# Optimization experiments

Measured on AMD Instinct MI355X. Metric: run time of the kernel, lower is better.

The kernel has to match this reference:

```python
import jax, jax.numpy as jnp
import numpy as np

N_HEAD = 16


def setup_inputs() -> dict:
    key = jax.random.key(0)
    ks = jax.random.split(key, 5)
    B, T, D_IN, D = 2, 2048, 1152, 1024
    s_in = 1.0 / np.sqrt(D_IN)
    s_d = 1.0 / np.sqrt(D)
    return {
        "xp": jax.random.normal(ks[0], (B, T, D_IN), jnp.float32),
        "Wq": jax.random.normal(ks[1], (D_IN, D), jnp.float32) * s_in,
        "bq": jnp.zeros((D,), jnp.float32),
        "Wk": jax.random.normal(ks[2], (D_IN, D), jnp.float32) * s_in,
        "bk": jnp.zeros((D,), jnp.float32),
        "Wv": jax.random.normal(ks[3], (D_IN, D), jnp.float32) * s_in,
        "bv": jnp.zeros((D,), jnp.float32),
        "Wp": jax.random.normal(ks[4], (D, D), jnp.float32) * s_d,
        "bp": jnp.zeros((D,), jnp.float32),
    }


def reference(xp, Wq, bq, Wk, bk, Wv, bv, Wp, bp):
    B, T, _ = xp.shape
    D = Wq.shape[1]
    hd = D // N_HEAD  # head dim
    # q, k, v projections -> [B, H, T, hd]
    def split_heads(t):
        return t.reshape(B, T, N_HEAD, hd).transpose(0, 2, 1, 3)
    q = split_heads(xp @ Wq + bq)
    k = split_heads(xp @ Wk + bk)
    v = split_heads(xp @ Wv + bv)
    scale = 1.0 / np.sqrt(hd).astype(np.float32)
    att = jnp.einsum("bhqd,bhkd->bhqk", q, k) * scale  # [B,H,T,T]
    causal = jnp.tril(jnp.ones((T, T), bool))
    att = jnp.where(causal[None, None], att, -jnp.inf)
    att = jax.nn.softmax(att, axis=-1)
    y = jnp.einsum("bhqk,bhkd->bhqd", att, v)  # [B,H,T,hd]
    y = y.transpose(0, 2, 1, 3).reshape(B, T, D)
    return y @ Wp + bp
```

## Files before the change

### kernel.cpp

```cpp
#include <hip/hip_runtime.h>
#include <hip/hip_bf16.h>

typedef __attribute__((ext_vector_type(8))) short bf16x8;
typedef __attribute__((ext_vector_type(4))) short bf16x4;
typedef __attribute__((ext_vector_type(4))) float f32x4;
typedef __attribute__((ext_vector_type(2))) unsigned int u32x2;

__device__ __forceinline__ void gload_lds16(const void* g, void* l) {
    __builtin_amdgcn_global_load_lds(
        (const __attribute__((address_space(1))) unsigned int*)g,
        (__attribute__((address_space(3))) unsigned int*)l, 16, 0, 0);
}

__device__ __forceinline__ unsigned int pk2(float x, float y) {
    union { __hip_bfloat16 h[2]; unsigned int u; } z;
    z.h[0] = __float2bfloat16(x); z.h[1] = __float2bfloat16(y);
    return z.u;
}

__device__ __forceinline__ f32x4 mfma_16x16x16(bf16x4 a, bf16x4 b, f32x4 c) {
#if __has_builtin(__builtin_amdgcn_mfma_f32_16x16x16bf16_1k)
    return __builtin_amdgcn_mfma_f32_16x16x16bf16_1k(a, b, c, 0, 0, 0);
#else
    f32x4 d = c;
    asm volatile("v_mfma_f32_16x16x16_bf16 %0, %1, %2, %0" : "+v"(d) : "v"(a), "v"(b));
    return d;
#endif
}

__global__ void k_cvt_bf16(const float* __restrict__ x, __hip_bfloat16* __restrict__ o, int n8) {
    int i = blockIdx.x * 256 + threadIdx.x;
    if (i >= n8) return;
    const float4* xp = (const float4*)(x + (size_t)i * 8);
    float4 a = xp[0], b = xp[1];
    union { __hip_bfloat16 h[8]; uint4 u; } tu;
    tu.h[0] = __float2bfloat16(a.x); tu.h[1] = __float2bfloat16(a.y);
    tu.h[2] = __float2bfloat16(a.z); tu.h[3] = __float2bfloat16(a.w);
    tu.h[4] = __float2bfloat16(b.x); tu.h[5] = __float2bfloat16(b.y);
    tu.h[6] = __float2bfloat16(b.z); tu.h[7] = __float2bfloat16(b.w);
    *(uint4*)(o + (size_t)i * 8) = tu.u;
}

__global__ void k_tr3(const float* __restrict__ s0, const float* __restrict__ s1,
                      const float* __restrict__ s2, __hip_bfloat16* __restrict__ dst,
                      int K, int N) {
    __shared__ float tile[32][33];
    const float* src = (blockIdx.z == 0) ? s0 : ((blockIdx.z == 1) ? s1 : s2);
    __hip_bfloat16* d = dst + (size_t)blockIdx.z * N * K;
    int n0 = blockIdx.x * 32, k0 = blockIdx.y * 32;
    int tx = threadIdx.x & 31, ty = threadIdx.x >> 5;
#pragma unroll
    for (int i = 0; i < 4; i++)
        tile[ty + i * 8][tx] = src[(size_t)(k0 + ty + i * 8) * N + n0 + tx];
    __syncthreads();
#pragma unroll
    for (int i = 0; i < 4; i++)
        d[(size_t)(n0 + ty + i * 8) * K + k0 + tx] = __float2bfloat16(tile[tx][ty + i * 8]);
}

__global__ void k_tr(const float* __restrict__ src, __hip_bfloat16* __restrict__ dst, int K, int N) {
    __shared__ float tile[32][33];
    int n0 = blockIdx.x * 32, k0 = blockIdx.y * 32;
    int tx = threadIdx.x & 31, ty = threadIdx.x >> 5;
#pragma unroll
    for (int i = 0; i < 4; i++)
        tile[ty + i * 8][tx] = src[(size_t)(k0 + ty + i * 8) * N + n0 + tx];
    __syncthreads();
#pragma unroll
    for (int i = 0; i < 4; i++)
        dst[(size_t)(n0 + ty + i * 8) * K + k0 + tx] = __float2bfloat16(tile[tx][ty + i * 8]);
}

#define QSCALE 0.18033688011111204f

template <int EPI>
__global__ __launch_bounds__(256, 2) void k_gemm(
    const __hip_bfloat16* __restrict__ A, const __hip_bfloat16* __restrict__ Bt,
    int M, int N, int K,
    const float* __restrict__ b0, const float* __restrict__ b1, const float* __restrict__ b2,
    __hip_bfloat16* __restrict__ qb, __hip_bfloat16* __restrict__ kb, __hip_bfloat16* __restrict__ vb,
    float* __restrict__ outp)
{
    __shared__ __align__(16) __hip_bfloat16 Sh[16384];
    __hip_bfloat16* As = Sh;
    __hip_bfloat16* Bs = Sh + 8192;
    const int t = threadIdx.x;
    const int lane = t & 63, w = t >> 6;
    const int wr = w >> 1, wc = w & 1;
    const int r16 = lane & 15, kg = lane >> 4;
    const int m0 = blockIdx.x * 128, n0 = blockIdx.y * 128;
    f32x4 acc[4][4] = {};
    const int ksteps = K >> 6;
    for (int kt = 0; kt < ksteps; ++kt) {
        if (kt) __syncthreads();
        const int ks = kt * 64;
#pragma unroll
        for (int i = 0; i < 4; i++) {
            int ci = i * 256 + t;
            int row = ci >> 3, kc = (ci & 7) * 8;
            gload_lds16(A + (size_t)(m0 + row) * K + ks + kc, As + ci * 8);
        }
#pragma unroll
        for (int i = 0; i < 4; i++) {
            int ci = i * 256 + t;
            int row = ci >> 3, kc = (ci & 7) * 8;
            gload_lds16(Bt + (size_t)(n0 + row) * K + ks + kc, Bs + ci * 8);
        }
        __syncthreads();
#pragma unroll
        for (int c = 0; c < 2; c++) {
            bf16x8 af[4], bfr[4];
#pragma unroll
            for (int mi = 0; mi < 4; mi++)
                af[mi] = *(const bf16x8*)(As + (wr * 64 + mi * 16 + r16) * 64 + c * 32 + kg * 8);
#pragma unroll
            for (int ni = 0; ni < 4; ni++)
                bfr[ni] = *(const bf16x8*)(Bs + (wc * 64 + ni * 16 + r16) * 64 + c * 32 + kg * 8);
#pragma unroll
            for (int mi = 0; mi < 4; mi++)
#pragma unroll
                for (int ni = 0; ni < 4; ni++)
                    acc[mi][ni] = __builtin_amdgcn_mfma_f32_16x16x32_bf16(af[mi], bfr[ni], acc[mi][ni], 0, 0, 0);
        }
    }
    if (EPI == 0 && n0 >= 2048) {
        __syncthreads();
#pragma unroll
        for (int mi = 0; mi < 4; mi++) {
#pragma unroll
            for (int ni = 0; ni < 4; ni++) {
                const int nl = wc * 64 + ni * 16 + r16;
                const int mb = wr * 64 + mi * 16 + kg * 4;
                const int r = n0 - 2048 + nl;
                const float bias = b2[r];
                u32x2 pk;
                pk[0] = pk2(acc[mi][ni][0] + bias, acc[mi][ni][1] + bias);
                pk[1] = pk2(acc[mi][ni][2] + bias, acc[mi][ni][3] + bias);
                *(u32x2*)(Sh + nl * 128 + (mb ^ ((nl & 7) << 3))) = pk;
            }
        }
        __syncthreads();
#pragma unroll
        for (int pass = 0; pass < 8; ++pass) {
            const int ci = pass * 256 + t;
            const int nl = ci >> 4;
            const int ms = (ci & 15) * 8;
            bf16x8 v = *(const bf16x8*)(Sh + nl * 128 + (ms ^ ((nl & 7) << 3)));
            const int r = n0 - 2048 + nl;
            const int hh = r >> 6, dd = r & 63;
            const int m = m0 + ms;
            const int bb = m >> 11, tt = m & 2047;
            *(bf16x8*)(vb + ((size_t)(bb * 16 + hh) * 64 + dd) * 2048 + tt) = v;
        }
        return;
    }
#pragma unroll
    for (int mi = 0; mi < 4; mi++) {
#pragma unroll
        for (int ni = 0; ni < 4; ni++) {
#pragma unroll
            for (int j = 0; j < 4; j++) {
                int m = m0 + wr * 64 + mi * 16 + kg * 4 + j;
                int n = n0 + wc * 64 + ni * 16 + r16;
                float val = acc[mi][ni][j];
                if (EPI == 0) {
                    int r = n & 1023;
                    int hh = r >> 6, dd = r & 63;
                    int bb = m >> 11, tt = m & 2047;
                    if (n < 1024) {
                        val = (val + b0[r]) * QSCALE;
                        qb[((size_t)(bb * 16 + hh) * 2048 + tt) * 64 + dd] = __float2bfloat16(val);
                    } else {
                        val += b1[r];
                        kb[((size_t)(bb * 16 + hh) * 2048 + tt) * 64 + dd] = __float2bfloat16(val);
                    }
                } else {
                    outp[(size_t)m * N + n] = val + b0[n];
                }
            }
        }
    }
}

__global__ __launch_bounds__(256, 4) void k_attn(
    const __hip_bfloat16* __restrict__ qbuf,
    const __hip_bfloat16* __restrict__ kbuf,
    const __hip_bfloat16* __restrict__ vtbuf,
    __hip_bfloat16* __restrict__ y)
{
    __shared__ __align__(16) __hip_bfloat16 Kl[2][64 * 64];
    __shared__ __align__(16) __hip_bfloat16 Vl[2][64 * 64];
    const int t = threadIdx.x, lane = t & 63, w = t >> 6;
    const int r16 = lane & 15, kg = lane >> 4;
    const int g = blockIdx.x;
    const int c4 = g >> 8, p = g & 255;
    const int bh = (p >> 5) * 4 + c4;
    const int rr = p & 31;
    const int qt = (c4 & 1) ? rr : 31 - rr;
    const int swr = (r16 & 7) << 3;
    const int q0 = qt * 64 + w * 16;
    const __hip_bfloat16* qp = qbuf + ((size_t)bh * 2048 + q0) * 64;
    bf16x8 qf0 = *(const bf16x8*)(qp + r16 * 64 + kg * 8);
    bf16x8 qf1 = *(const bf16x8*)(qp + r16 * 64 + 32 + kg * 8);
    f32x4 O[4] = {};
    float m_s = -3.0e38f, l_s = 0.f;
    const __hip_bfloat16* kb = kbuf + (size_t)bh * 2048 * 64;
    const __hip_bfloat16* vb = vtbuf + (size_t)bh * 64 * 2048;

    const int ci0 = t, ci1 = 256 + t;
    const int kr0 = ci0 >> 3, sc0 = ((ci0 & 7) * 8) ^ ((kr0 & 7) << 3);
    const int kr1 = ci1 >> 3, sc1 = ((ci1 & 7) * 8) ^ ((kr1 & 7) << 3);

    gload_lds16(kb + (size_t)kr0 * 64 + sc0, &Kl[0][ci0 * 8]);
    gload_lds16(kb + (size_t)kr1 * 64 + sc1, &Kl[0][ci1 * 8]);
    gload_lds16(vb + (size_t)kr0 * 2048 + sc0, &Vl[0][ci0 * 8]);
    gload_lds16(vb + (size_t)kr1 * 2048 + sc1, &Vl[0][ci1 * 8]);
    __syncthreads();

    for (int kt = 0; kt <= qt; ++kt) {
        const int cur = kt & 1;
        if (kt < qt) {
            const int kn = kt + 1;
            gload_lds16(kb + (size_t)kn * 4096 + (size_t)kr0 * 64 + sc0, &Kl[cur ^ 1][ci0 * 8]);
            gload_lds16(kb + (size_t)kn * 4096 + (size_t)kr1 * 64 + sc1, &Kl[cur ^ 1][ci1 * 8]);
            gload_lds16(vb + (size_t)kr0 * 2048 + kn * 64 + sc0, &Vl[cur ^ 1][ci0 * 8]);
            gload_lds16(vb + (size_t)kr1 * 2048 + kn * 64 + sc1, &Vl[cur ^ 1][ci1 * 8]);
        }
        const int kbase = kt * 64;
        if (kbase <= q0 + 15) {
            const __hip_bfloat16* Klb = Kl[cur];
            const __hip_bfloat16* Vlb = Vl[cur];
            f32x4 S[4];
            __builtin_amdgcn_s_setprio(1);
#pragma unroll
            for (int ct = 0; ct < 4; ct++) {
                f32x4 s = {};
                const int r = ct * 16 + r16;
                bf16x8 kf0 = *(const bf16x8*)(Klb + r * 64 + ((kg * 8) ^ swr));
                s = __builtin_amdgcn_mfma_f32_16x16x32_bf16(kf0, qf0, s, 0, 0, 0);
                bf16x8 kf1 = *(const bf16x8*)(Klb + r * 64 + ((32 + kg * 8) ^ swr));
                s = __builtin_amdgcn_mfma_f32_16x16x32_bf16(kf1, qf1, s, 0, 0, 0);
                S[ct] = s;
            }
            __builtin_amdgcn_s_setprio(0);
            if (kbase + 63 > q0) {
#pragma unroll
                for (int ct = 0; ct < 4; ct++)
#pragma unroll
                    for (int j = 0; j < 4; j++)
                        if (kbase + ct * 16 + kg * 4 + j > q0 + r16) S[ct][j] = -3.0e38f;
            }
            float rmax = S[0][0];
#pragma unroll
            for (int ct = 0; ct < 4; ct++)
#pragma unroll
                for (int j = 0; j < 4; j++) rmax = fmaxf(rmax, S[ct][j]);
            rmax = fmaxf(rmax, __shfl_xor(rmax, 16));
            rmax = fmaxf(rmax, __shfl_xor(rmax, 32));
            if (__any(rmax > m_s + 8.0f)) {
                const float mn = fmaxf(m_s, rmax);
                const float al = exp2f(m_s - mn);
                m_s = mn;
                l_s *= al;
#pragma unroll
                for (int j = 0; j < 4; j++) {
                    const float aj = __shfl(al, kg * 4 + j);
#pragma unroll
                    for (int ot = 0; ot < 4; ot++) O[ot][j] *= aj;
                }
            }
            float rsum = 0.f;
#pragma unroll
            for (int ct = 0; ct < 4; ct++)
#pragma unroll
                for (int j = 0; j < 4; j++) { S[ct][j] = exp2f(S[ct][j] - m_s); rsum += S[ct][j]; }
            rsum += __shfl_xor(rsum, 16);
            rsum += __shfl_xor(rsum, 32);
            l_s += rsum;
            bf16x4 pa[4];
#pragma unroll
            for (int ct = 0; ct < 4; ct++) {
                union { __hip_bfloat16 h[4]; bf16x4 v; } pk;
                pk.h[0] = __float2bfloat16(S[ct][0]);
                pk.h[1] = __float2bfloat16(S[ct][1]);
                pk.h[2] = __float2bfloat16(S[ct][2]);
                pk.h[3] = __float2bfloat16(S[ct][3]);
                pa[ct] = pk.v;
            }
            __builtin_amdgcn_s_setprio(1);
#pragma unroll
            for (int ot = 0; ot < 4; ot++) {
                const int vrow = ot * 16 + r16;
#pragma unroll
                for (int ct = 0; ct < 4; ct++) {
                    bf16x4 vf = *(const bf16x4*)(Vlb + vrow * 64 + ((ct * 16 + kg * 4) ^ ((vrow & 7) << 3)));
                    O[ot] = mfma_16x16x16(pa[ct], vf, O[ot]);
                }
            }
            __builtin_amdgcn_s_setprio(0);
        }
        __syncthreads();
    }
    const int b = bh >> 4, h = bh & 15;
    const float linv = 1.0f / l_s;
#pragma unroll
    for (int j = 0; j < 4; j++) {
        const float iv = __shfl(linv, kg * 4 + j);
        const int qq = q0 + kg * 4 + j;
#pragma unroll
        for (int ot = 0; ot < 4; ot++)
            y[((size_t)b * 2048 + qq) * 1024 + h * 64 + ot * 16 + r16] = __float2bfloat16(O[ot][j] * iv);
    }
}

extern "C" void kernel_launch(void* const* d_in, const int* in_sizes, int n_in,
                              void* d_out, int out_size, void* d_ws, size_t ws_size,
                              hipStream_t stream) {
    const float* xp = (const float*)d_in[0];
    const float* Wq = (const float*)d_in[1];
    const float* bq = (const float*)d_in[2];
    const float* Wk = (const float*)d_in[3];
    const float* bk = (const float*)d_in[4];
    const float* Wv = (const float*)d_in[5];
    const float* bv = (const float*)d_in[6];
    const float* Wp = (const float*)d_in[7];
    const float* bp = (const float*)d_in[8];
    float* out = (float*)d_out;

    char* ws = (char*)d_ws;
    __hip_bfloat16* xb     = (__hip_bfloat16*)(ws);
    __hip_bfloat16* Wqkv_t = (__hip_bfloat16*)(ws + 9437184);
    __hip_bfloat16* Wp_t   = (__hip_bfloat16*)(ws + 16515072);
    __hip_bfloat16* qb     = (__hip_bfloat16*)(ws + 18612224);
    __hip_bfloat16* kbv    = (__hip_bfloat16*)(ws + 27000832);
    __hip_bfloat16* vtb    = (__hip_bfloat16*)(ws + 35389440);
    __hip_bfloat16* yb     = (__hip_bfloat16*)(ws + 43778048);

    k_cvt_bf16<<<2304, 256, 0, stream>>>(xp, xb, 589824);
    dim3 trg3(1024 / 32, 1152 / 32, 3);
    k_tr3<<<trg3, 256, 0, stream>>>(Wq, Wk, Wv, Wqkv_t, 1152, 1024);
    dim3 trg2(1024 / 32, 1024 / 32);
    k_tr<<<trg2, 256, 0, stream>>>(Wp, Wp_t, 1024, 1024);

    dim3 g1(4096 / 128, 3072 / 128);
    k_gemm<0><<<g1, 256, 0, stream>>>(xb, Wqkv_t, 4096, 3072, 1152, bq, bk, bv, qb, kbv, vtb, nullptr);
    k_attn<<<1024, 256, 0, stream>>>(qb, kbv, vtb, yb);
    dim3 g2(4096 / 128, 1024 / 128);
    k_gemm<1><<<g2, 256, 0, stream>>>(yb, Wp_t, 4096, 1024, 1024, bp, nullptr, nullptr,
                                      nullptr, nullptr, nullptr, out);
}
```

Measured before the change: 137.3 us.

## Remap GEMM and attention block indices so each XCD works on a contiguous L2 region

Both GEMMs move from a 2D grid to a 1D grid. Each block index is decoded so that blocks scheduled round-robin onto the same XCD (bid&7) cover one contiguous M×N sub-grid, which improves per-XCD L2 reuse of the A and B tiles. The attention kernel is remapped the same way, so that all q-tiles of a set of heads share an XCD and its K/V stay in that L2. It also removes the per-wave skip check for fully masked key tiles, so some waves compute fully masked tiles instead of skipping them.

New measurement: 138.1 us. No clear change (+0.6%).

```diff
diff --git a/kernel.cpp b/kernel.cpp
--- a/kernel.cpp
+++ b/kernel.cpp
@@ -79,7 +79,7 @@
     int M, int N, int K,
     const float* __restrict__ b0, const float* __restrict__ b1, const float* __restrict__ b2,
     __hip_bfloat16* __restrict__ qb, __hip_bfloat16* __restrict__ kb, __hip_bfloat16* __restrict__ vb,
-    float* __restrict__ outp)
+    float* __restrict__ outp, int cm, int cn)
 {
     __shared__ __align__(16) __hip_bfloat16 Sh[16384];
     __hip_bfloat16* As = Sh;
@@ -88,21 +88,26 @@
     const int lane = t & 63, w = t >> 6;
     const int wr = w >> 1, wc = w & 1;
     const int r16 = lane & 15, kg = lane >> 4;
-    const int m0 = blockIdx.x * 128, n0 = blockIdx.y * 128;
+    const int bid = blockIdx.x;
+    const int xcd = bid & 7;
+    const int mc = xcd >> 1, nc = xcd & 1;
+    const int i = bid >> 3;
+    const int ml = i % cm, nl = i / cm;
+    const int m0 = (mc * cm + ml) * 128, n0 = (nc * cn + nl) * 128;
     f32x4 acc[4][4] = {};
     const int ksteps = K >> 6;
     for (int kt = 0; kt < ksteps; ++kt) {
         if (kt) __syncthreads();
         const int ks = kt * 64;
 #pragma unroll
-        for (int i = 0; i < 4; i++) {
-            int ci = i * 256 + t;
+        for (int i2 = 0; i2 < 4; i2++) {
+            int ci = i2 * 256 + t;
             int row = ci >> 3, kc = (ci & 7) * 8;
             gload_lds16(A + (size_t)(m0 + row) * K + ks + kc, As + ci * 8);
         }
 #pragma unroll
-        for (int i = 0; i < 4; i++) {
-            int ci = i * 256 + t;
+        for (int i2 = 0; i2 < 4; i2++) {
+            int ci = i2 * 256 + t;
             int row = ci >> 3, kc = (ci & 7) * 8;
             gload_lds16(Bt + (size_t)(n0 + row) * K + ks + kc, Bs + ci * 8);
         }
@@ -129,24 +134,24 @@
         for (int mi = 0; mi < 4; mi++) {
 #pragma unroll
             for (int ni = 0; ni < 4; ni++) {
-                const int nl = wc * 64 + ni * 16 + r16;
+                const int nl2 = wc * 64 + ni * 16 + r16;
                 const int mb = wr * 64 + mi * 16 + kg * 4;
-                const int r = n0 - 2048 + nl;
+                const int r = n0 - 2048 + nl2;
                 const float bias = b2[r];
                 u32x2 pk;
                 pk[0] = pk2(acc[mi][ni][0] + bias, acc[mi][ni][1] + bias);
                 pk[1] = pk2(acc[mi][ni][2] + bias, acc[mi][ni][3] + bias);
-                *(u32x2*)(Sh + nl * 128 + (mb ^ ((nl & 7) << 3))) = pk;
+                *(u32x2*)(Sh + nl2 * 128 + (mb ^ ((nl2 & 7) << 3))) = pk;
             }
         }
         __syncthreads();
 #pragma unroll
         for (int pass = 0; pass < 8; ++pass) {
             const int ci = pass * 256 + t;
-            const int nl = ci >> 4;
+            const int nl2 = ci >> 4;
             const int ms = (ci & 15) * 8;
-            bf16x8 v = *(const bf16x8*)(Sh + nl * 128 + (ms ^ ((nl & 7) << 3)));
-            const int r = n0 - 2048 + nl;
+            bf16x8 v = *(const bf16x8*)(Sh + nl2 * 128 + (ms ^ ((nl2 & 7) << 3)));
+            const int r = n0 - 2048 + nl2;
             const int hh = r >> 6, dd = r & 63;
             const int m = m0 + ms;
             const int bb = m >> 11, tt = m & 2047;
@@ -193,10 +198,10 @@
     const int t = threadIdx.x, lane = t & 63, w = t >> 6;
     const int r16 = lane & 15, kg = lane >> 4;
     const int g = blockIdx.x;
-    const int c4 = g >> 8, p = g & 255;
-    const int bh = (p >> 5) * 4 + c4;
-    const int rr = p & 31;
-    const int qt = (c4 & 1) ? rr : 31 - rr;
+    const int xcd = g & 7, idx = g >> 3;
+    const int j4 = idx >> 5, rr = idx & 31;
+    const int bh = xcd * 4 + j4;
+    const int qt = (j4 & 1) ? rr : 31 - rr;
     const int swr = (r16 & 7) << 3;
     const int q0 = qt * 64 + w * 16;
     const __hip_bfloat16* qp = qbuf + ((size_t)bh * 2048 + q0) * 64;
@@ -227,7 +232,7 @@
             gload_lds16(vb + (size_t)kr1 * 2048 + kn * 64 + sc1, &Vl[cur ^ 1][ci1 * 8]);
         }
         const int kbase = kt * 64;
-        if (kbase <= q0 + 15) {
+        {
             const __hip_bfloat16* Klb = Kl[cur];
             const __hip_bfloat16* Vlb = Vl[cur];
             f32x4 S[4];
@@ -342,10 +347,9 @@
     dim3 trg2(1024 / 32, 1024 / 32);
     k_tr<<<trg2, 256, 0, stream>>>(Wp, Wp_t, 1024, 1024);
 
-    dim3 g1(4096 / 128, 3072 / 128);
-    k_gemm<0><<<g1, 256, 0, stream>>>(xb, Wqkv_t, 4096, 3072, 1152, bq, bk, bv, qb, kbv, vtb, nullptr);
+    k_gemm<0><<<768, 256, 0, stream>>>(xb, Wqkv_t, 4096, 3072, 1152, bq, bk, bv, qb, kbv, vtb,
+                                       nullptr, 8, 12);
     k_attn<<<1024, 256, 0, stream>>>(qb, kbv, vtb, yb);
-    dim3 g2(4096 / 128, 1024 / 128);
-    k_gemm<1><<<g2, 256, 0, stream>>>(yb, Wp_t, 4096, 1024, 1024, bp, nullptr, nullptr,
-                                      nullptr, nullptr, nullptr, out);
-}
+    k_gemm<1><<<256, 256, 0, stream>>>(yb, Wp_t, 4096, 1024, 1024, bp, nullptr, nullptr,
+                                       nullptr, nullptr, nullptr, out, 8, 4);
+}
```

## Add 8-wave 256x256 double-buffered QKV GEMM and XCD-aware attention block mapping

Applied to the files above, without the earlier changes.

Replaces the QKV projection GEMM with a new 512-thread kernel using 256x256 tiles, double-buffered swizzled LDS, and an interleaved schedule of LDS reads, async global-to-LDS loads and MFMA quadrants, with manual waitcnt and barriers. The aim is to hide global load latency and raise data reuse per block, at the cost of more LDS use and fewer blocks (192 for the grid). The attention block index is remapped so each XCD handles contiguous heads for better L2 locality, and the per-wave causal skip check is removed. The output projection GEMM is split into its own simpler kernel.

Result: slower. 149.1 us (+8.6%).

```diff
diff --git a/kernel.cpp b/kernel.cpp
--- a/kernel.cpp
+++ b/kernel.cpp
@@ -27,6 +27,11 @@
     return d;
 #endif
 }
+
+#define BARRIER() asm volatile("s_barrier" ::: "memory")
+#define LGKM0()   asm volatile("s_waitcnt lgkmcnt(0)" ::: "memory")
+#define VM2()     asm volatile("s_waitcnt vmcnt(2)" ::: "memory")
+#define VM0()     asm volatile("s_waitcnt vmcnt(0)" ::: "memory")
 
 __global__ void k_cvt_bf16(const float* __restrict__ x, __hip_bfloat16* __restrict__ o, int n8) {
     int i = blockIdx.x * 256 + threadIdx.x;
@@ -73,17 +78,191 @@
 
 #define QSCALE 0.18033688011111204f
 
-template <int EPI>
-__global__ __launch_bounds__(256, 2) void k_gemm(
+__device__ __forceinline__ void read_af(const __hip_bfloat16* base, int wm, int mh, int r16,
+                                        int kg, int swr, bf16x8 af[4][2]) {
+#pragma unroll
+    for (int mf = 0; mf < 4; ++mf)
+#pragma unroll
+        for (int kc = 0; kc < 2; ++kc) {
+            const int row = wm * 128 + (mh * 4 + mf) * 16 + r16;
+            af[mf][kc] = *(const bf16x8*)(base + row * 64 + ((kc * 32 + kg * 8) ^ swr));
+        }
+}
+__device__ __forceinline__ void read_bf(const __hip_bfloat16* base, int wn, int nh, int r16,
+                                        int kg, int swr, bf16x8 bfr[2][2]) {
+#pragma unroll
+    for (int nf = 0; nf < 2; ++nf)
+#pragma unroll
+        for (int kc = 0; kc < 2; ++kc) {
+            const int row = wn * 64 + (nh * 2 + nf) * 16 + r16;
+            bfr[nf][kc] = *(const bf16x8*)(base + row * 64 + ((kc * 32 + kg * 8) ^ swr));
+        }
+}
+__device__ __forceinline__ void mfma_q(f32x4 (&acc)[8][4], bf16x8 af[4][2], bf16x8 bfr[2][2],
+                                       int mh, int nh) {
+#pragma unroll
+    for (int mf = 0; mf < 4; ++mf)
+#pragma unroll
+        for (int nf = 0; nf < 2; ++nf)
+#pragma unroll
+            for (int kc = 0; kc < 2; ++kc)
+                acc[mh * 4 + mf][nh * 2 + nf] = __builtin_amdgcn_mfma_f32_16x16x32_bf16(
+                    af[mf][kc], bfr[nf][kc], acc[mh * 4 + mf][nh * 2 + nf], 0, 0, 0);
+}
+
+__global__ __launch_bounds__(512, 2) void k_gemm8(
+    const __hip_bfloat16* __restrict__ A, const __hip_bfloat16* __restrict__ Bt, int K,
+    const float* __restrict__ b0, const float* __restrict__ b1, const float* __restrict__ b2,
+    __hip_bfloat16* __restrict__ qb, __hip_bfloat16* __restrict__ kb, __hip_bfloat16* __restrict__ vb)
+{
+    __shared__ __align__(16) __hip_bfloat16 Al[2][256 * 64];
+    __shared__ __align__(16) __hip_bfloat16 Bl[2][256 * 64];
+    const int t = threadIdx.x;
+    const int lane = t & 63, wid = t >> 6;
+    const int r16 = lane & 15, kg = lane >> 4;
+    const int wm = wid >> 2, wn = wid & 3;
+    const int m0 = blockIdx.x * 256, n0 = blockIdx.y * 256;
+    const int swr = (r16 & 7) << 3;
+
+    const int ci0 = t, ci1 = 512 + t;
+    const int sr0 = ci0 >> 3, sc0 = ((ci0 & 7) * 8) ^ ((sr0 & 7) << 3);
+    const int sr1 = ci1 >> 3, sc1 = ((ci1 & 7) * 8) ^ ((sr1 & 7) << 3);
+
+    auto stA = [&](int b, int h, int kt) {
+        gload_lds16(A + (size_t)(m0 + h * 128 + sr0) * K + kt * 64 + sc0, &Al[b][h * 8192 + ci0 * 8]);
+        gload_lds16(A + (size_t)(m0 + h * 128 + sr1) * K + kt * 64 + sc1, &Al[b][h * 8192 + ci1 * 8]);
+    };
+    auto stB = [&](int b, int h, int kt) {
+        gload_lds16(Bt + (size_t)(n0 + h * 128 + sr0) * K + kt * 64 + sc0, &Bl[b][h * 8192 + ci0 * 8]);
+        gload_lds16(Bt + (size_t)(n0 + h * 128 + sr1) * K + kt * 64 + sc1, &Bl[b][h * 8192 + ci1 * 8]);
+    };
+
+    f32x4 acc[8][4] = {};
+    const int nkt = K >> 6, niter = nkt >> 1;
+
+    stA(0, 0, 0); stA(0, 1, 0); stB(0, 0, 0); stB(0, 1, 0);
+    stA(1, 0, 1);
+    VM2(); BARRIER();
+
+    for (int it = 0; it < niter; ++it) {
+        const int t1 = 2 * it + 1;
+        const bool last = (it == niter - 1);
+        bf16x8 af[4][2], bfr[2][2];
+        read_af(Al[0], wm, 0, r16, kg, swr, af);
+        read_bf(Bl[0], wn, 0, r16, kg, swr, bfr);
+        stA(1, 1, t1);
+        BARRIER(); LGKM0();
+        __builtin_amdgcn_s_setprio(1); mfma_q(acc, af, bfr, 0, 0); __builtin_amdgcn_s_setprio(0);
+        BARRIER();
+        read_bf(Bl[0], wn, 1, r16, kg, swr, bfr);
+        stB(1, 0, t1);
+        BARRIER(); LGKM0();
+        __builtin_amdgcn_s_setprio(1); mfma_q(acc, af, bfr, 0, 1); __builtin_amdgcn_s_setprio(0);
+        BARRIER();
+        read_af(Al[0], wm, 1, r16, kg, swr, af);
+        read_bf(Bl[0], wn, 0, r16, kg, swr, bfr);
+        stB(1, 1, t1);
+        BARRIER(); LGKM0();
+        __builtin_amdgcn_s_setprio(1); mfma_q(acc, af, bfr, 1, 0); __builtin_amdgcn_s_setprio(0);
+        BARRIER();
+        read_bf(Bl[0], wn, 1, r16, kg, swr, bfr);
+        if (!last) stA(0, 0, t1 + 1);
+        BARRIER(); LGKM0();
+        __builtin_amdgcn_s_setprio(1); mfma_q(acc, af, bfr, 1, 1); __builtin_amdgcn_s_setprio(0);
+        if (last) { VM0(); } else { VM2(); }
+        BARRIER();
+        read_af(Al[1], wm, 0, r16, kg, swr, af);
+        read_bf(Bl[1], wn, 0, r16, kg, swr, bfr);
+        if (!last) stA(0, 1, t1 + 1);
+        BARRIER(); LGKM0();
+        __builtin_amdgcn_s_setprio(1); mfma_q(acc, af, bfr, 0, 0); __builtin_amdgcn_s_setprio(0);
+        BARRIER();
+        read_bf(Bl[1], wn, 1, r16, kg, swr, bfr);
+        if (!last) stB(0, 0, t1 + 1);
+        BARRIER(); LGKM0();
+        __builtin_amdgcn_s_setprio(1); mfma_q(acc, af, bfr, 0, 1); __builtin_amdgcn_s_setprio(0);
+        BARRIER();
+        read_af(Al[1], wm, 1, r16, kg, swr, af);
+        read_bf(Bl[1], wn, 0, r16, kg, swr, bfr);
+        if (!last) stB(0, 1, t1 + 1);
+        BARRIER(); LGKM0();
+        __builtin_amdgcn_s_setprio(1); mfma_q(acc, af, bfr, 1, 0); __builtin_amdgcn_s_setprio(0);
+        BARRIER();
+        read_bf(Bl[1], wn, 1, r16, kg, swr, bfr);
+        if (!last) stA(1, 0, t1 + 2);
+        BARRIER(); LGKM0();
+        __builtin_amdgcn_s_setprio(1); mfma_q(acc, af, bfr, 1, 1); __builtin_amdgcn_s_setprio(0);
+        if (!last) { VM2(); }
+        BARRIER();
+    }
+
+    if (n0 >= 2048) {
+        __hip_bfloat16* Alf = &Al[0][0];
+        __hip_bfloat16* Blf = &Bl[0][0];
+        __syncthreads();
+        __hip_bfloat16* dst = wm ? Blf : Alf;
+#pragma unroll
+        for (int mf = 0; mf < 8; ++mf) {
+#pragma unroll
+            for (int nf = 0; nf < 4; ++nf) {
+                const int nl = wn * 64 + nf * 16 + r16;
+                const int mp = mf * 16 + kg * 4;
+                const float bias = b2[n0 - 2048 + nl];
+                u32x2 pk;
+                pk[0] = pk2(acc[mf][nf][0] + bias, acc[mf][nf][1] + bias);
+                pk[1] = pk2(acc[mf][nf][2] + bias, acc[mf][nf][3] + bias);
+                *(u32x2*)(dst + nl * 128 + (mp ^ ((nl & 7) << 3))) = pk;
+            }
+        }
+        __syncthreads();
+#pragma unroll
+        for (int h = 0; h < 2; ++h) {
+            const __hip_bfloat16* src = h ? Blf : Alf;
+#pragma unroll
+            for (int pass = 0; pass < 8; ++pass) {
+                const int ci = pass * 512 + t;
+                const int nl = ci >> 4;
+                const int ms = (ci & 15) * 8;
+                bf16x8 v = *(const bf16x8*)(src + nl * 128 + (ms ^ ((nl & 7) << 3)));
+                const int r = n0 - 2048 + nl;
+                const int hh = r >> 6, dd = r & 63;
+                const int m = m0 + h * 128 + ms;
+                const int bb = m >> 11, tt = m & 2047;
+                *(bf16x8*)(vb + ((size_t)(bb * 16 + hh) * 64 + dd) * 2048 + tt) = v;
+            }
+        }
+        return;
+    }
+#pragma unroll
+    for (int mf = 0; mf < 8; ++mf) {
+#pragma unroll
+        for (int nf = 0; nf < 4; ++nf) {
+#pragma unroll
+            for (int j = 0; j < 4; ++j) {
+                const int m = m0 + wm * 128 + mf * 16 + kg * 4 + j;
+                const int n = n0 + wn * 64 + nf * 16 + r16;
+                const int r = n & 1023;
+                const int hh = r >> 6, dd = r & 63;
+                const int bb = m >> 11, tt = m & 2047;
+                float val = acc[mf][nf][j];
+                if (n0 < 1024) {
+                    val = (val + b0[r]) * QSCALE;
+                    qb[((size_t)(bb * 16 + hh) * 2048 + tt) * 64 + dd] = __float2bfloat16(val);
+                } else {
+                    val += b1[r];
+                    kb[((size_t)(bb * 16 + hh) * 2048 + tt) * 64 + dd] = __float2bfloat16(val);
+                }
+            }
+        }
+    }
+}
+
+__global__ __launch_bounds__(256, 2) void k_gemmP(
     const __hip_bfloat16* __restrict__ A, const __hip_bfloat16* __restrict__ Bt,
-    int M, int N, int K,
-    const float* __restrict__ b0, const float* __restrict__ b1, const float* __restrict__ b2,
-    __hip_bfloat16* __restrict__ qb, __hip_bfloat16* __restrict__ kb, __hip_bfloat16* __restrict__ vb,
-    float* __restrict__ outp)
+    int N, int K, const float* __restrict__ bias, float* __restrict__ outp)
 {
-    __shared__ __align__(16) __hip_bfloat16 Sh[16384];
-    __hip_bfloat16* As = Sh;
-    __hip_bfloat16* Bs = Sh + 8192;
+    __shared__ __align__(16) __hip_bfloat16 As[128 * 64];
+    __shared__ __align__(16) __hip_bfloat16 Bs[128 * 64];
     const int t = threadIdx.x;
     const int lane = t & 63, w = t >> 6;
     const int wr = w >> 1, wc = w & 1;
@@ -123,63 +302,16 @@
                     acc[mi][ni] = __builtin_amdgcn_mfma_f32_16x16x32_bf16(af[mi], bfr[ni], acc[mi][ni], 0, 0, 0);
         }
     }
-    if (EPI == 0 && n0 >= 2048) {
-        __syncthreads();
-#pragma unroll
-        for (int mi = 0; mi < 4; mi++) {
-#pragma unroll
-            for (int ni = 0; ni < 4; ni++) {
-                const int nl = wc * 64 + ni * 16 + r16;
-                const int mb = wr * 64 + mi * 16 + kg * 4;
-                const int r = n0 - 2048 + nl;
-                const float bias = b2[r];
-                u32x2 pk;
-                pk[0] = pk2(acc[mi][ni][0] + bias, acc[mi][ni][1] + bias);
-                pk[1] = pk2(acc[mi][ni][2] + bias, acc[mi][ni][3] + bias);
-                *(u32x2*)(Sh + nl * 128 + (mb ^ ((nl & 7) << 3))) = pk;
-            }
-        }
-        __syncthreads();
-#pragma unroll
-        for (int pass = 0; pass < 8; ++pass) {
-            const int ci = pass * 256 + t;
-            const int nl = ci >> 4;
-            const int ms = (ci & 15) * 8;
-            bf16x8 v = *(const bf16x8*)(Sh + nl * 128 + (ms ^ ((nl & 7) << 3)));
-            const int r = n0 - 2048 + nl;
-            const int hh = r >> 6, dd = r & 63;
-            const int m = m0 + ms;
-            const int bb = m >> 11, tt = m & 2047;
-            *(bf16x8*)(vb + ((size_t)(bb * 16 + hh) * 64 + dd) * 2048 + tt) = v;
-        }
-        return;
-    }
-#pragma unroll
-    for (int mi = 0; mi < 4; mi++) {
-#pragma unroll
-        for (int ni = 0; ni < 4; ni++) {
+#pragma unroll
+    for (int mi = 0; mi < 4; mi++)
+#pragma unroll
+        for (int ni = 0; ni < 4; ni++)
 #pragma unroll
             for (int j = 0; j < 4; j++) {
                 int m = m0 + wr * 64 + mi * 16 + kg * 4 + j;
                 int n = n0 + wc * 64 + ni * 16 + r16;
-                float val = acc[mi][ni][j];
-                if (EPI == 0) {
-                    int r = n & 1023;
-                    int hh = r >> 6, dd = r & 63;
-                    int bb = m >> 11, tt = m & 2047;
-                    if (n < 1024) {
-                        val = (val + b0[r]) * QSCALE;
-                        qb[((size_t)(bb * 16 + hh) * 2048 + tt) * 64 + dd] = __float2bfloat16(val);
-                    } else {
-                        val += b1[r];
-                        kb[((size_t)(bb * 16 + hh) * 2048 + tt) * 64 + dd] = __float2bfloat16(val);
-                    }
-                } else {
-                    outp[(size_t)m * N + n] = val + b0[n];
-                }
-            }
-        }
-    }
+                outp[(size_t)m * N + n] = acc[mi][ni][j] + bias[n];
+            }
 }
 
 __global__ __launch_bounds__(256, 4) void k_attn(
@@ -193,10 +325,10 @@
     const int t = threadIdx.x, lane = t & 63, w = t >> 6;
     const int r16 = lane & 15, kg = lane >> 4;
     const int g = blockIdx.x;
-    const int c4 = g >> 8, p = g & 255;
-    const int bh = (p >> 5) * 4 + c4;
-    const int rr = p & 31;
-    const int qt = (c4 & 1) ? rr : 31 - rr;
+    const int xcd = g & 7, idx = g >> 3;
+    const int j4 = idx >> 5, rr = idx & 31;
+    const int bh = xcd * 4 + j4;
+    const int qt = (j4 & 1) ? rr : 31 - rr;
     const int swr = (r16 & 7) << 3;
     const int q0 = qt * 64 + w * 16;
     const __hip_bfloat16* qp = qbuf + ((size_t)bh * 2048 + q0) * 64;
@@ -227,7 +359,7 @@
             gload_lds16(vb + (size_t)kr1 * 2048 + kn * 64 + sc1, &Vl[cur ^ 1][ci1 * 8]);
         }
         const int kbase = kt * 64;
-        if (kbase <= q0 + 15) {
+        {
             const __hip_bfloat16* Klb = Kl[cur];
             const __hip_bfloat16* Vlb = Vl[cur];
             f32x4 S[4];
@@ -342,10 +474,9 @@
     dim3 trg2(1024 / 32, 1024 / 32);
     k_tr<<<trg2, 256, 0, stream>>>(Wp, Wp_t, 1024, 1024);
 
-    dim3 g1(4096 / 128, 3072 / 128);
-    k_gemm<0><<<g1, 256, 0, stream>>>(xb, Wqkv_t, 4096, 3072, 1152, bq, bk, bv, qb, kbv, vtb, nullptr);
+    dim3 g8(4096 / 256, 3072 / 256);
+    k_gemm8<<<g8, 512, 0, stream>>>(xb, Wqkv_t, 1152, bq, bk, bv, qb, kbv, vtb);
     k_attn<<<1024, 256, 0, stream>>>(qb, kbv, vtb, yb);
-    dim3 g2(4096 / 128, 1024 / 128);
-    k_gemm<1><<<g2, 256, 0, stream>>>(yb, Wp_t, 4096, 1024, 1024, bp, nullptr, nullptr,
-                                      nullptr, nullptr, nullptr, out);
-}
+    dim3 gp(4096 / 128, 1024 / 128);
+    k_gemmP<<<gp, 256, 0, stream>>>(yb, Wp_t, 1024, 1024, bp, out);
+}
```
